# Performance work log

Measured on AMD Instinct MI355X. Metric: run time of the kernel, lower is better.

The kernel has to match this reference:

```python
import jax, jax.numpy as jnp
import numpy as np

NUM_LAYERS, CHANNELS, IN_CHANNELS = 3, 8, 8
MASK_OUT_STRIDE = 4
SOI = np.array([64., 128., 256., 512., 1024.], dtype=np.float32)  # sizes_of_interest + [last*2]
WEIGHT_NUMS = [(IN_CHANNELS + 2) * CHANNELS, CHANNELS * CHANNELS, CHANNELS * 1]
BIAS_NUMS = [CHANNELS, CHANNELS, 1]
NUM_GEN_PARAMS = sum(WEIGHT_NUMS) + sum(BIAS_NUMS)  # 169


def aligned_bilinear(t, factor):
    # Faithful port of adet.utils.comm.aligned_bilinear (align_corners=True).
    if factor == 1:
        return t
    n, c, h, w = t.shape
    t = jnp.pad(t, ((0, 0), (0, 0), (0, 1), (0, 1)), mode='edge')  # replicate pad right/bottom
    oh, ow = factor * h + 1, factor * w + 1

    def interp_axis(x, out_len, axis):
        # align_corners=True with scale exactly 1/factor -> src = out_idx / factor
        src = jnp.arange(out_len) / factor
        i0 = jnp.floor(src).astype(jnp.int32)
        i1 = jnp.minimum(i0 + 1, x.shape[axis] - 1)
        frac = (src - i0).astype(x.dtype)
        x0 = jnp.take(x, i0, axis=axis)
        x1 = jnp.take(x, i1, axis=axis)
        shp = [1] * x.ndim
        shp[axis] = out_len
        frac = frac.reshape(shp)
        return x0 * (1 - frac) + x1 * frac

    t = interp_axis(t, oh, 2)
    t = interp_axis(t, ow, 3)
    p = factor // 2
    t = jnp.pad(t, ((0, 0), (0, 0), (p, 0), (p, 0)), mode='edge')
    return t[:, :, :oh - 1, :ow - 1]  # final size (factor*h, factor*w)


def parse_dynamic_params(params):
    # params: [n_inst, 169] -> per-layer weights [n, c_out, c_in] and biases [n, c_out]
    n = params.shape[0]
    sizes = WEIGHT_NUMS + BIAS_NUMS
    offs = np.cumsum([0] + sizes)
    splits = [params[:, offs[i]:offs[i + 1]] for i in range(len(sizes))]
    w_splits, b_splits = splits[:NUM_LAYERS], splits[NUM_LAYERS:]
    weights, biases = [], []
    for l in range(NUM_LAYERS):
        c_out = CHANNELS if l < NUM_LAYERS - 1 else 1
        weights.append(w_splits[l].reshape(n, c_out, -1))
        biases.append(b_splits[l].reshape(n, c_out))
    return weights, biases


def setup_inputs():
    key = jax.random.key(0)
    k1, k2, k3, k4, k5 = jax.random.split(key, 5)
    N, C, H, W = 2, IN_CHANNELS, 128, 192
    n_inst = 128
    stride = 8
    return {
        'mask_feats': jax.random.normal(k1, (N, C, H, W), jnp.float32),
        'mask_head_params': jax.random.normal(k2, (n_inst, NUM_GEN_PARAMS), jnp.float32) * 0.1,
        'instance_locations': jax.random.uniform(k3, (n_inst, 2), jnp.float32)
                              * jnp.array([W * stride, H * stride], jnp.float32),  # pixel coords (x, y)
        'im_inds': jax.random.randint(k4, (n_inst,), 0, N),
        'fpn_levels': jax.random.randint(k5, (n_inst,), 0, 5),
        'mask_feat_stride': stride,
    }


def reference(mask_feats, mask_head_params, instance_locations, im_inds, fpn_levels, mask_feat_stride):
    N, C, H, W = mask_feats.shape
    n_inst = mask_head_params.shape[0]
    s = mask_feat_stride

    # compute_locations: (x, y) pixel centers of the stride-s grid, [H*W, 2]
    sx = jnp.arange(W, dtype=jnp.float32) * s + s // 2
    sy = jnp.arange(H, dtype=jnp.float32) * s + s // 2
    yy, xx = jnp.meshgrid(sy, sx, indexing='ij')
    locations = jnp.stack([xx.ravel(), yy.ravel()], axis=1)  # [HW, 2]

    # relative coords, normalized by size-of-interest of the instance's FPN level
    rel = instance_locations[:, None, :] - locations[None, :, :]        # [n, HW, 2]
    rel = jnp.transpose(rel, (0, 2, 1))                                  # [n, 2, HW]
    soi = jnp.asarray(SOI)[fpn_levels]                                   # [n]
    rel = (rel / soi[:, None, None]).astype(mask_feats.dtype)

    feats = mask_feats[im_inds].reshape(n_inst, C, H * W)                # [n, C, HW]
    x = jnp.concatenate([rel, feats], axis=1)                            # [n, C+2, HW]

    weights, biases = parse_dynamic_params(mask_head_params)
    # grouped 1x1 convs == per-instance tiny GEMM chain with ReLUs
    for l in range(NUM_LAYERS):
        x = jnp.einsum('noi,nih->noh', weights[l], x) + biases[l][:, :, None]
        if l < NUM_LAYERS - 1:
            x = jax.nn.relu(x)

    mask_logits = x.reshape(n_inst, 1, H, W)
    factor = mask_feat_stride // MASK_OUT_STRIDE
    return aligned_bilinear(mask_logits, factor)  # [n_inst, 1, 2H, 2W]
```

## Files before the change

### kernel.cpp

```cpp
#include <hip/hip_runtime.h>

#define C_IN   8
#define CH     8
#define Hh     128
#define Ww     192
#define HW     (Hh*Ww)
#define NINST  128
#define NPAR   169
#define OH     256
#define OW     384
#define B      4
#define RT     (B+1)
#define NRG    (Hh/B)

typedef float f32x2 __attribute__((ext_vector_type(2)));
typedef float f32x4 __attribute__((ext_vector_type(4)));

__device__ __forceinline__ f32x2 pk2(float s) { f32x2 r; r.x = s; r.y = s; return r; }


__global__ __launch_bounds__(192, 3)
void fused_maskhead_kernel(const float* __restrict__ feats,
                           const float* __restrict__ params,
                           const float* __restrict__ locs,
                           const int* __restrict__ im_inds,
                           const int* __restrict__ fpn,
                           float* __restrict__ out)
{
    __shared__ __align__(16) float sw[192];
    __shared__ float sl[RT][Ww];

    const int rg   = blockIdx.x;
    const int inst = blockIdx.y;
    const int x    = threadIdx.x;
    const int r0   = rg * B;

    if (x < NPAR) {
        const int r = x;
        int dst;
        if (r < 80)       { const int o = r / 10; dst = o * 12 + (r - o * 10); }
        else if (r < 144) dst = 96  + (r - 80);
        else if (r < 152) dst = 160 + (r - 144);
        else if (r < 160) dst = 168 + (r - 152);
        else if (r < 168) dst = 176 + (r - 160);
        else              dst = 184;
        sw[dst] = params[inst * NPAR + r];
    }

    const float ixv = locs[inst * 2 + 0];
    const float iyv = locs[inst * 2 + 1];
    const float inv_soi = 1.0f / (float)(64 << fpn[inst]);
    const float rx = (ixv - (float)(x * 8 + 4)) * inv_soi;
    const float* fb = feats + (size_t)im_inds[inst] * (C_IN * HW) + x;
    const int sr4 = min(r0 + 4, Hh - 1);

    f32x2 ry2[2];
    ry2[0].x = (iyv - (float)((r0 + 0) * 8 + 4)) * inv_soi;
    ry2[0].y = (iyv - (float)((r0 + 1) * 8 + 4)) * inv_soi;
    ry2[1].x = (iyv - (float)((r0 + 2) * 8 + 4)) * inv_soi;
    ry2[1].y = (iyv - (float)((r0 + 3) * 8 + 4)) * inv_soi;
    const float ry4 = (iyv - (float)(sr4 * 8 + 4)) * inv_soi;

    f32x2 f2[2][C_IN];
    float f4[C_IN];
    #pragma unroll
    for (int c = 0; c < C_IN; ++c) {
        const float* fc = fb + c * HW;
        f2[0][c].x = fc[(r0 + 0) * Ww];
        f2[0][c].y = fc[(r0 + 1) * Ww];
        f2[1][c].x = fc[(r0 + 2) * Ww];
        f2[1][c].y = fc[(r0 + 3) * Ww];
        f4[c]      = fc[sr4 * Ww];
    }

    __syncthreads();

    f32x2 h1a[CH], h1b[CH];
    float h1s[CH];
    #pragma unroll
    for (int o = 0; o < CH; ++o) {
        const f32x4 wa = *(const f32x4*)(sw + o * 12 + 0);
        const f32x4 wb = *(const f32x4*)(sw + o * 12 + 4);
        const f32x4 wc = *(const f32x4*)(sw + o * 12 + 8);
        const float c0 = fmaf(wa.x, rx, sw[168 + o]);
        const float wv[C_IN] = {wa.z, wa.w, wb.x, wb.y, wb.z, wb.w, wc.x, wc.y};

        f32x2 a0 = pk2(wa.y) * ry2[0] + pk2(c0);
        f32x2 a1 = pk2(wa.y) * ry2[1] + pk2(c0);
        float a4 = fmaf(wa.y, ry4, c0);
        #pragma unroll
        for (int c = 0; c < C_IN; ++c) {
            a0 = pk2(wv[c]) * f2[0][c] + a0;
            a1 = pk2(wv[c]) * f2[1][c] + a1;
            a4 = fmaf(wv[c], f4[c], a4);
        }
        h1a[o].x = fmaxf(a0.x, 0.0f);  h1a[o].y = fmaxf(a0.y, 0.0f);
        h1b[o].x = fmaxf(a1.x, 0.0f);  h1b[o].y = fmaxf(a1.y, 0.0f);
        h1s[o]   = fmaxf(a4, 0.0f);
    }

    f32x2 h2a[CH], h2b[CH];
    float h2s[CH];
    #pragma unroll
    for (int o = 0; o < CH; ++o) {
        const f32x4 wa = *(const f32x4*)(sw + 96 + o * 8 + 0);
        const f32x4 wb = *(const f32x4*)(sw + 96 + o * 8 + 4);
        const float bo = sw[176 + o];
        const float wv[CH] = {wa.x, wa.y, wa.z, wa.w, wb.x, wb.y, wb.z, wb.w};

        f32x2 a0 = pk2(bo);
        f32x2 a1 = pk2(bo);
        float a4 = bo;
        #pragma unroll
        for (int c = 0; c < CH; ++c) {
            a0 = pk2(wv[c]) * h1a[c] + a0;
            a1 = pk2(wv[c]) * h1b[c] + a1;
            a4 = fmaf(wv[c], h1s[c], a4);
        }
        h2a[o].x = fmaxf(a0.x, 0.0f);  h2a[o].y = fmaxf(a0.y, 0.0f);
        h2b[o].x = fmaxf(a1.x, 0.0f);  h2b[o].y = fmaxf(a1.y, 0.0f);
        h2s[o]   = fmaxf(a4, 0.0f);
    }

    {
        const f32x4 wa = *(const f32x4*)(sw + 160);
        const f32x4 wb = *(const f32x4*)(sw + 164);
        const float bo = sw[184];
        const float wv[CH] = {wa.x, wa.y, wa.z, wa.w, wb.x, wb.y, wb.z, wb.w};

        f32x2 z0 = pk2(bo);
        f32x2 z1 = pk2(bo);
        float z4 = bo;
        #pragma unroll
        for (int c = 0; c < CH; ++c) {
            z0 = pk2(wv[c]) * h2a[c] + z0;
            z1 = pk2(wv[c]) * h2b[c] + z1;
            z4 = fmaf(wv[c], h2s[c], z4);
        }
        sl[0][x] = z0.x;
        sl[1][x] = z0.y;
        sl[2][x] = z1.x;
        sl[3][x] = z1.y;
        sl[4][x] = z4;
    }

    __syncthreads();

    f32x2* outf2 = (f32x2*)out;
    const int xm1 = max(x - 1, 0);
    const int jlo = (rg == 0) ? -2 : 0;
    const int jhi = (rg == NRG - 1) ? 2 * B - 2 : 2 * B;

    #pragma unroll 4
    for (int jj = jlo; jj < jhi; ++jj) {
        const int oy  = 2 * r0 + 2 + jj;
        const int ay  = max(oy - 1, 0);
        const int y0l = (ay >> 1) - r0;
        const int y1l = min(y0l + 1, B);
        const float fy = (ay & 1) ? 0.5f : 0.0f;

        const float t01 = sl[y0l][x];
        const float t00 = sl[y0l][xm1];
        const float t11 = sl[y1l][x];
        const float t10 = sl[y1l][xm1];

        const float rma = fmaf(fy, t10 - t00, t00);
        const float rmb = fmaf(fy, t11 - t01, t01);

        f32x2 v;
        v.x = 0.5f * (rma + rmb);
        v.y = rmb;
        outf2[((size_t)inst * OH + oy) * (OW / 2) + x] = v;
    }
}

extern "C" void kernel_launch(void* const* d_in, const int* in_sizes, int n_in,
                              void* d_out, int out_size, void* d_ws, size_t ws_size,
                              hipStream_t stream) {
    const float* feats  = (const float*)d_in[0];
    const float* params = (const float*)d_in[1];
    const float* locs   = (const float*)d_in[2];
    const int*   im     = (const int*)d_in[3];
    const int*   fpn    = (const int*)d_in[4];
    float* out = (float*)d_out;

    dim3 grid(NRG, NINST);
    fused_maskhead_kernel<<<grid, 192, 0, stream>>>(feats, params, locs, im, fpn, out);
}
```

Baseline: 28.30 us.

## Split fused mask head into MLP kernel and separate upsample kernel

Breaks the single fused kernel into two. The first runs the per-instance MLP and writes the logits to workspace. The second reads them back to do the bilinear upsample, with one float4 store per thread. This drops the extra halo row of MLP work per block, the LDS staging and the second barrier. In exchange it adds a global round-trip of the logits (about 12.6 MB written and read) and a second kernel launch.

```diff
diff --git a/kernel.cpp b/kernel.cpp
--- a/kernel.cpp
+++ b/kernel.cpp
@@ -10,7 +10,6 @@
 #define OH     256
 #define OW     384
 #define B      4
-#define RT     (B+1)
 #define NRG    (Hh/B)
 
 typedef float f32x2 __attribute__((ext_vector_type(2)));
@@ -20,15 +19,14 @@
 
 
 __global__ __launch_bounds__(192, 3)
-void fused_maskhead_kernel(const float* __restrict__ feats,
-                           const float* __restrict__ params,
-                           const float* __restrict__ locs,
-                           const int* __restrict__ im_inds,
-                           const int* __restrict__ fpn,
-                           float* __restrict__ out)
+void mlp_kernel(const float* __restrict__ feats,
+                const float* __restrict__ params,
+                const float* __restrict__ locs,
+                const int* __restrict__ im_inds,
+                const int* __restrict__ fpn,
+                float* __restrict__ logits)
 {
     __shared__ __align__(16) float sw[192];
-    __shared__ float sl[RT][Ww];
 
     const int rg   = blockIdx.x;
     const int inst = blockIdx.y;
@@ -52,17 +50,14 @@
     const float inv_soi = 1.0f / (float)(64 << fpn[inst]);
     const float rx = (ixv - (float)(x * 8 + 4)) * inv_soi;
     const float* fb = feats + (size_t)im_inds[inst] * (C_IN * HW) + x;
-    const int sr4 = min(r0 + 4, Hh - 1);
 
     f32x2 ry2[2];
     ry2[0].x = (iyv - (float)((r0 + 0) * 8 + 4)) * inv_soi;
     ry2[0].y = (iyv - (float)((r0 + 1) * 8 + 4)) * inv_soi;
     ry2[1].x = (iyv - (float)((r0 + 2) * 8 + 4)) * inv_soi;
     ry2[1].y = (iyv - (float)((r0 + 3) * 8 + 4)) * inv_soi;
-    const float ry4 = (iyv - (float)(sr4 * 8 + 4)) * inv_soi;
 
     f32x2 f2[2][C_IN];
-    float f4[C_IN];
     #pragma unroll
     for (int c = 0; c < C_IN; ++c) {
         const float* fc = fb + c * HW;
@@ -70,13 +65,11 @@
         f2[0][c].y = fc[(r0 + 1) * Ww];
         f2[1][c].x = fc[(r0 + 2) * Ww];
         f2[1][c].y = fc[(r0 + 3) * Ww];
-        f4[c]      = fc[sr4 * Ww];
     }
 
     __syncthreads();
 
     f32x2 h1a[CH], h1b[CH];
-    float h1s[CH];
     #pragma unroll
     for (int o = 0; o < CH; ++o) {
         const f32x4 wa = *(const f32x4*)(sw + o * 12 + 0);
@@ -87,20 +80,16 @@
 
         f32x2 a0 = pk2(wa.y) * ry2[0] + pk2(c0);
         f32x2 a1 = pk2(wa.y) * ry2[1] + pk2(c0);
-        float a4 = fmaf(wa.y, ry4, c0);
         #pragma unroll
         for (int c = 0; c < C_IN; ++c) {
             a0 = pk2(wv[c]) * f2[0][c] + a0;
             a1 = pk2(wv[c]) * f2[1][c] + a1;
-            a4 = fmaf(wv[c], f4[c], a4);
         }
         h1a[o].x = fmaxf(a0.x, 0.0f);  h1a[o].y = fmaxf(a0.y, 0.0f);
         h1b[o].x = fmaxf(a1.x, 0.0f);  h1b[o].y = fmaxf(a1.y, 0.0f);
-        h1s[o]   = fmaxf(a4, 0.0f);
     }
 
     f32x2 h2a[CH], h2b[CH];
-    float h2s[CH];
     #pragma unroll
     for (int o = 0; o < CH; ++o) {
         const f32x4 wa = *(const f32x4*)(sw + 96 + o * 8 + 0);
@@ -110,16 +99,13 @@
 
         f32x2 a0 = pk2(bo);
         f32x2 a1 = pk2(bo);
-        float a4 = bo;
         #pragma unroll
         for (int c = 0; c < CH; ++c) {
             a0 = pk2(wv[c]) * h1a[c] + a0;
             a1 = pk2(wv[c]) * h1b[c] + a1;
-            a4 = fmaf(wv[c], h1s[c], a4);
         }
         h2a[o].x = fmaxf(a0.x, 0.0f);  h2a[o].y = fmaxf(a0.y, 0.0f);
         h2b[o].x = fmaxf(a1.x, 0.0f);  h2b[o].y = fmaxf(a1.y, 0.0f);
-        h2s[o]   = fmaxf(a4, 0.0f);
     }
 
     {
@@ -130,48 +116,54 @@
 
         f32x2 z0 = pk2(bo);
         f32x2 z1 = pk2(bo);
-        float z4 = bo;
         #pragma unroll
         for (int c = 0; c < CH; ++c) {
             z0 = pk2(wv[c]) * h2a[c] + z0;
             z1 = pk2(wv[c]) * h2b[c] + z1;
-            z4 = fmaf(wv[c], h2s[c], z4);
         }
-        sl[0][x] = z0.x;
-        sl[1][x] = z0.y;
-        sl[2][x] = z1.x;
-        sl[3][x] = z1.y;
-        sl[4][x] = z4;
+        float* lp = logits + ((size_t)inst * Hh + r0) * Ww + x;
+        lp[0 * Ww] = z0.x;
+        lp[1 * Ww] = z0.y;
+        lp[2 * Ww] = z1.x;
+        lp[3 * Ww] = z1.y;
     }
+}
 
-    __syncthreads();
+__global__ __launch_bounds__(256)
+void upsample_kernel(const float* __restrict__ logits, f32x4* __restrict__ out)
+{
+    const int idx  = blockIdx.x * 256 + threadIdx.x;
+    const int g    = idx % (OW / 4);
+    const int r    = idx / (OW / 4);
+    const int oy   = r % OH;
+    const int inst = r / OH;
 
-    f32x2* outf2 = (f32x2*)out;
-    const int xm1 = max(x - 1, 0);
-    const int jlo = (rg == 0) ? -2 : 0;
-    const int jhi = (rg == NRG - 1) ? 2 * B - 2 : 2 * B;
+    const float* L = logits + (size_t)inst * HW;
 
-    #pragma unroll 4
-    for (int jj = jlo; jj < jhi; ++jj) {
-        const int oy  = 2 * r0 + 2 + jj;
-        const int ay  = max(oy - 1, 0);
-        const int y0l = (ay >> 1) - r0;
-        const int y1l = min(y0l + 1, B);
-        const float fy = (ay & 1) ? 0.5f : 0.0f;
+    const int ay = max(oy - 1, 0);
+    const int y0 = ay >> 1;
+    const int y1 = min(y0 + 1, Hh - 1);
+    const float fy = (ay & 1) ? 0.5f : 0.0f;
 
-        const float t01 = sl[y0l][x];
-        const float t00 = sl[y0l][xm1];
-        const float t11 = sl[y1l][x];
-        const float t10 = sl[y1l][xm1];
+    const int m0  = 2 * g;
+    const int mm1 = max(m0 - 1, 0);
+    const int mp1 = m0 + 1;
 
-        const float rma = fmaf(fy, t10 - t00, t00);
-        const float rmb = fmaf(fy, t11 - t01, t01);
+    const float* La = L + y0 * Ww;
+    const float* Lb = L + y1 * Ww;
+    const float a0 = La[mm1], a1 = La[m0], a2 = La[mp1];
+    const float b0 = Lb[mm1], b1 = Lb[m0], b2 = Lb[mp1];
 
-        f32x2 v;
-        v.x = 0.5f * (rma + rmb);
-        v.y = rmb;
-        outf2[((size_t)inst * OH + oy) * (OW / 2) + x] = v;
-    }
+    const float r0v = fmaf(fy, b0 - a0, a0);
+    const float r1v = fmaf(fy, b1 - a1, a1);
+    const float r2v = fmaf(fy, b2 - a2, a2);
+
+    f32x4 v;
+    v.x = 0.5f * (r0v + r1v);
+    v.y = r1v;
+    v.z = 0.5f * (r1v + r2v);
+    v.w = r2v;
+    out[idx] = v;
 }
 
 extern "C" void kernel_launch(void* const* d_in, const int* in_sizes, int n_in,
@@ -182,8 +174,12 @@
     const float* locs   = (const float*)d_in[2];
     const int*   im     = (const int*)d_in[3];
     const int*   fpn    = (const int*)d_in[4];
-    float* out = (float*)d_out;
+    float* out    = (float*)d_out;
+    float* logits = (float*)d_ws;
 
-    dim3 grid(NRG, NINST);
-    fused_maskhead_kernel<<<grid, 192, 0, stream>>>(feats, params, locs, im, fpn, out);
+    dim3 g1(NRG, NINST);
+    mlp_kernel<<<g1, 192, 0, stream>>>(feats, params, locs, im, fpn, logits);
+
+    const int nf4 = NINST * OH * (OW / 4);
+    upsample_kernel<<<nf4 / 256, 256, 0, stream>>>(logits, (f32x4*)out);
 }
```

After: 37.40 us. 1.32x slower.

## Fuse final layer into layer-2 loop and exchange logits via wave shuffles

Applied to the files above, without the earlier changes.

Folds the last 8-to-1 layer into the layer-2 loop, so layer-2 activations are accumulated directly into the output logit instead of being held in register arrays. The per-block LDS logit tile is replaced by __shfl_up to get the left neighbour's values, with a tiny LDS buffer only for the lanes at wave boundaries. The upsampling loop becomes fully unrolled with precomputed row blends, and the first two output rows get a special case. The aim is lower register pressure and less LDS traffic. The cost is added dependence on the 64-wide wave layout and extra boundary logic.

```diff
diff --git a/kernel.cpp b/kernel.cpp
--- a/kernel.cpp
+++ b/kernel.cpp
@@ -10,7 +10,6 @@
 #define OH     256
 #define OW     384
 #define B      4
-#define RT     (B+1)
 #define NRG    (Hh/B)
 
 typedef float f32x2 __attribute__((ext_vector_type(2)));
@@ -28,7 +27,7 @@
                            float* __restrict__ out)
 {
     __shared__ __align__(16) float sw[192];
-    __shared__ float sl[RT][Ww];
+    __shared__ float sb[2][5];
 
     const int rg   = blockIdx.x;
     const int inst = blockIdx.y;
@@ -99,13 +98,15 @@
         h1s[o]   = fmaxf(a4, 0.0f);
     }
 
-    f32x2 h2a[CH], h2b[CH];
-    float h2s[CH];
+    f32x2 z01 = pk2(sw[184]);
+    f32x2 z23 = pk2(sw[184]);
+    float z4v = sw[184];
     #pragma unroll
     for (int o = 0; o < CH; ++o) {
         const f32x4 wa = *(const f32x4*)(sw + 96 + o * 8 + 0);
         const f32x4 wb = *(const f32x4*)(sw + 96 + o * 8 + 4);
         const float bo = sw[176 + o];
+        const float w2o = sw[160 + o];
         const float wv[CH] = {wa.x, wa.y, wa.z, wa.w, wb.x, wb.y, wb.z, wb.w};
 
         f32x2 a0 = pk2(bo);
@@ -117,60 +118,51 @@
             a1 = pk2(wv[c]) * h1b[c] + a1;
             a4 = fmaf(wv[c], h1s[c], a4);
         }
-        h2a[o].x = fmaxf(a0.x, 0.0f);  h2a[o].y = fmaxf(a0.y, 0.0f);
-        h2b[o].x = fmaxf(a1.x, 0.0f);  h2b[o].y = fmaxf(a1.y, 0.0f);
-        h2s[o]   = fmaxf(a4, 0.0f);
+        f32x2 t0, t1;
+        t0.x = fmaxf(a0.x, 0.0f);  t0.y = fmaxf(a0.y, 0.0f);
+        t1.x = fmaxf(a1.x, 0.0f);  t1.y = fmaxf(a1.y, 0.0f);
+        z01 = pk2(w2o) * t0 + z01;
+        z23 = pk2(w2o) * t1 + z23;
+        z4v = fmaf(w2o, fmaxf(a4, 0.0f), z4v);
     }
 
-    {
-        const f32x4 wa = *(const f32x4*)(sw + 160);
-        const f32x4 wb = *(const f32x4*)(sw + 164);
-        const float bo = sw[184];
-        const float wv[CH] = {wa.x, wa.y, wa.z, wa.w, wb.x, wb.y, wb.z, wb.w};
+    const float z0 = z01.x, z1 = z01.y, z2 = z23.x, z3 = z23.y, z4 = z4v;
 
-        f32x2 z0 = pk2(bo);
-        f32x2 z1 = pk2(bo);
-        float z4 = bo;
-        #pragma unroll
-        for (int c = 0; c < CH; ++c) {
-            z0 = pk2(wv[c]) * h2a[c] + z0;
-            z1 = pk2(wv[c]) * h2b[c] + z1;
-            z4 = fmaf(wv[c], h2s[c], z4);
-        }
-        sl[0][x] = z0.x;
-        sl[1][x] = z0.y;
-        sl[2][x] = z1.x;
-        sl[3][x] = z1.y;
-        sl[4][x] = z4;
-    }
-
+    if (x == 63)  { sb[0][0]=z0; sb[0][1]=z1; sb[0][2]=z2; sb[0][3]=z3; sb[0][4]=z4; }
+    if (x == 127) { sb[1][0]=z0; sb[1][1]=z1; sb[1][2]=z2; sb[1][3]=z3; sb[1][4]=z4; }
     __syncthreads();
 
+    float zp0 = __shfl_up(z0, 1);
+    float zp1 = __shfl_up(z1, 1);
+    float zp2 = __shfl_up(z2, 1);
+    float zp3 = __shfl_up(z3, 1);
+    float zp4 = __shfl_up(z4, 1);
+    if (x == 64)  { zp0=sb[0][0]; zp1=sb[0][1]; zp2=sb[0][2]; zp3=sb[0][3]; zp4=sb[0][4]; }
+    if (x == 128) { zp0=sb[1][0]; zp1=sb[1][1]; zp2=sb[1][2]; zp3=sb[1][3]; zp4=sb[1][4]; }
+
+    const float rmb[8] = { 0.5f*(z0+z1), z1, 0.5f*(z1+z2), z2,
+                           0.5f*(z2+z3), z3, 0.5f*(z3+z4), z4 };
+    const float rma[8] = { 0.5f*(zp0+zp1), zp1, 0.5f*(zp1+zp2), zp2,
+                           0.5f*(zp2+zp3), zp3, 0.5f*(zp3+zp4), zp4 };
+
     f32x2* outf2 = (f32x2*)out;
-    const int xm1 = max(x - 1, 0);
-    const int jlo = (rg == 0) ? -2 : 0;
-    const int jhi = (rg == NRG - 1) ? 2 * B - 2 : 2 * B;
-
-    #pragma unroll 4
-    for (int jj = jlo; jj < jhi; ++jj) {
-        const int oy  = 2 * r0 + 2 + jj;
-        const int ay  = max(oy - 1, 0);
-        const int y0l = (ay >> 1) - r0;
-        const int y1l = min(y0l + 1, B);
-        const float fy = (ay & 1) ? 0.5f : 0.0f;
-
-        const float t01 = sl[y0l][x];
-        const float t00 = sl[y0l][xm1];
-        const float t11 = sl[y1l][x];
-        const float t10 = sl[y1l][xm1];
-
-        const float rma = fmaf(fy, t10 - t00, t00);
-        const float rmb = fmaf(fy, t11 - t01, t01);
-
+    const size_t obase = ((size_t)inst * OH + (2 * r0 + 2)) * (OW / 2) + x;
+    #pragma unroll
+    for (int j = 0; j < 8; ++j) {
+        if (rg < NRG - 1 || j < 6) {
+            f32x2 v;
+            v.x = 0.5f * (rma[j] + rmb[j]);
+            v.y = rmb[j];
+            outf2[obase + (size_t)j * (OW / 2)] = v;
+        }
+    }
+    if (rg == 0) {
         f32x2 v;
-        v.x = 0.5f * (rma + rmb);
-        v.y = rmb;
-        outf2[((size_t)inst * OH + oy) * (OW / 2) + x] = v;
+        v.x = 0.5f * (zp0 + z0);
+        v.y = z0;
+        const size_t e = (size_t)inst * OH * (OW / 2) + x;
+        outf2[e] = v;
+        outf2[e + (OW / 2)] = v;
     }
 }
 
```

Result: faster. 27.43 us (-3.1%).
